# Kernel tuning notes

Measured on AMD Instinct MI355X. Metric: run time of the kernel, lower is better.

The kernel has to match this reference:

```python
import jax, jax.numpy as jnp
import numpy as np

B, T, D, H = 1024, 128, 128, 256

def _uni(k, shape, fan):
    s = 1.0 / np.sqrt(fan)
    return jax.random.uniform(k, shape, jnp.float32, -s, s)

def setup_inputs():
    key = jax.random.key(0)
    ks = jax.random.split(key, 22)
    inp = {}
    inp['x'] = jax.random.normal(ks[0], (B, T, D), jnp.float32)
    inp['x_hat'] = jax.random.normal(ks[1], (B, T, D), jnp.float32)
    inp['u'] = jax.random.uniform(ks[2], (B, T, D), jnp.float32)
    inp['m'] = (jax.random.uniform(ks[3], (B, T, D)) < 0.8).astype(jnp.float32)
    inp['d'] = jax.random.uniform(ks[4], (B, T, D), jnp.float32)
    # Decay(D -> H)
    inp['W_decay'] = _uni(ks[5], (H, D), D)
    inp['b_decay'] = _uni(ks[6], (H,), D)
    # hist: Linear(H -> D)
    inp['W_hist'] = _uni(ks[7], (D, H), H)
    inp['b_hist'] = _uni(ks[8], (D,), H)
    inp['Wv'] = _uni(ks[9], (D, D), D)
    inp['bv'] = _uni(ks[10], (D,), D)
    inp['Wr'] = _uni(ks[11], (D, D), D)
    inp['br'] = _uni(ks[12], (D,), D)
    # Conv1d(2,1,kernel=1) == learned 2-way combine
    inp['conv_w'] = _uni(ks[13], (2,), 2)
    inp['conv_b'] = _uni(ks[14], (), 2)
    # GRUCell(2*D -> H), torch layout [3H, in] rows = (r, z, n)
    inp['W_ih'] = _uni(ks[15], (3 * H, 2 * D), 2 * D)
    inp['W_hh'] = _uni(ks[16], (3 * H, H), H)
    inp['b_ih'] = _uni(ks[17], (3 * H,), H)
    inp['b_hh'] = _uni(ks[18], (3 * H,), H)
    # fc_out: Linear(H -> 1)
    inp['W_out'] = _uni(ks[19], (1, H), H)
    inp['b_out'] = _uni(ks[20], (1,), H)
    return inp

def reference(x, x_hat, u, m, d, W_decay, b_decay, W_hist, b_hist, Wv, bv, Wr, br,
              conv_w, conv_b, W_ih, W_hh, b_ih, b_hh, W_out, b_out):
    off = 1.0 - jnp.eye(D, dtype=x.dtype)
    # Precompute everything that does not depend on the recurrent state h:
    gamma = jnp.exp(-jax.nn.relu(jnp.einsum('btd,hd->bth', d, W_decay) + b_decay))  # [B,T,H]
    xbar = m * x + (1.0 - m) * x_hat
    xu = jnp.einsum('btd,ed->bte', xbar, Wv * off) + bv  # [B,T,D] (unc_flag == 0 path)
    Wr_m = Wr * off

    def step(carry, inp):
        h, loss = carry
        x_t, m_t, g_t, xu_t = inp  # [B,D],[B,D],[B,H],[B,D]
        h = h * g_t
        x_h = h @ W_hist.T + b_hist
        x_r = m_t * x_t + (1.0 - m_t) * x_h
        xr = x_r @ Wr_m.T + br
        x_comb = conv_w[0] * xu_t + conv_w[1] * xr + conv_b  # Conv1d(2,1,1)
        loss = loss + jnp.sum(jnp.abs(x_t - x_comb) * m_t) / (jnp.sum(m_t) + 1e-5)
        x_imp = m_t * x_t + (1.0 - m_t) * x_comb
        gin = jnp.concatenate([x_imp, m_t], axis=1)  # [B, 2D]
        gi = gin @ W_ih.T + b_ih
        gh = h @ W_hh.T + b_hh
        i_r, i_z, i_n = jnp.split(gi, 3, axis=1)
        h_r, h_z, h_n = jnp.split(gh, 3, axis=1)
        r = jax.nn.sigmoid(i_r + h_r)
        z = jax.nn.sigmoid(i_z + h_z)
        n = jnp.tanh(i_n + r * h_n)
        h_new = (1.0 - z) * n + z * h
        return (h_new, loss), (x_imp, xr)

    h0 = jnp.zeros((B, H), x.dtype)
    xs = (jnp.swapaxes(x, 0, 1), jnp.swapaxes(m, 0, 1),
          jnp.swapaxes(gamma, 0, 1), jnp.swapaxes(xu, 0, 1))
    (h_fin, x_loss), (x_imp_t, xr_t) = jax.lax.scan(step, (h0, jnp.float32(0.0)), xs)
    x_imp = jnp.swapaxes(x_imp_t, 0, 1)  # [B,T,D]
    xrs = jnp.swapaxes(xr_t, 0, 1)
    y_out = h_fin @ W_out.T + b_out  # task == 'C', get_y == True
    y_score = jax.nn.sigmoid(y_out)
    return (x_imp, y_out, y_score, x_loss, xu, xrs)
```

## Files before the change

### kernel.cpp

```cpp
#include <hip/hip_runtime.h>
#include <math.h>

#define BQ 1024
#define TT 128
#define DD 128
#define HH 256
#define NW 8
#define NTH 512
#define NBLK 64

typedef float f32x4 __attribute__((ext_vector_type(4)));
typedef __bf16 bf16x8 __attribute__((ext_vector_type(8)));
typedef unsigned short u16x4 __attribute__((ext_vector_type(4)));
typedef unsigned short u16x8 __attribute__((ext_vector_type(8)));
typedef unsigned int u32x4 __attribute__((ext_vector_type(4)));
typedef unsigned int u32x2 __attribute__((ext_vector_type(2)));
typedef long long i64;

#define WS_MSUMF 8192
#define WS_WQ8   40960
#define WS_WB16  487424
#define WS_SA1   589824
#define WS_SA2   67698688

#define TQ_TOT  864

#define TB_DEC 0
#define TB_WV  64
#define TB_TOT 96

#define L_WX  0
#define L_HI  98304
#define L_WR  131072
#define L_HF8 147456
#define L_XRF 151552
#define L_XIF 153600
#define L_RED 155648
#define L_TOT 155712

__device__ __forceinline__ unsigned short f2bf(float f){
  union { float f; unsigned u; } v; v.f = f;
  unsigned r = v.u + 0x7FFFu + ((v.u >> 16) & 1u);
  return (unsigned short)(r >> 16);
}
__device__ __forceinline__ float sigm(float v){ return 1.f/(1.f + __expf(-v)); }
__device__ __forceinline__ float tanhfast(float v){ return 2.f*sigm(2.f*v) - 1.f; }
__device__ __forceinline__ unsigned pk4(float a, float b, float c, float d){
  int v = __builtin_amdgcn_cvt_pk_fp8_f32(a, b, 0, false);
  v = __builtin_amdgcn_cvt_pk_fp8_f32(c, d, v, true);
  return (unsigned)v;
}
__device__ __forceinline__ f32x4 upk4(unsigned w){
  f32x4 r;
  r[0] = __builtin_amdgcn_cvt_f32_fp8((int)w, 0);
  r[1] = __builtin_amdgcn_cvt_f32_fp8((int)w, 1);
  r[2] = __builtin_amdgcn_cvt_f32_fp8((int)w, 2);
  r[3] = __builtin_amdgcn_cvt_f32_fp8((int)w, 3);
  return r;
}
__device__ __forceinline__ f32x4 mfma8(i64 a, i64 b, f32x4 c){
  return __builtin_amdgcn_mfma_f32_16x16x32_fp8_fp8(a, b, c, 0, 0, 0);
}
__device__ __forceinline__ f32x4 mfma16b(bf16x8 a, bf16x8 b, f32x4 c){
  return __builtin_amdgcn_mfma_f32_16x16x32_bf16(a, b, c, 0, 0, 0);
}

__global__ void pack_w8(const float* Whh, const float* Wih, const float* Whist,
                        const float* Wr, unsigned char* wq){
  int gt = blockIdx.x*4 + (threadIdx.x>>6);
  int lane = threadIdx.x & 63;
  if (gt >= TQ_TOT) return;
  int lr = lane & 15, lg = lane >> 4;
  const float* src; int n, k0, K; int dm = 0;
  if (gt < 384){ int kt = gt & 7, gnt = gt >> 3;
    n = (gnt>>4)*256 + (gnt&15)*16 + lr; k0 = kt*32 + lg*8; src = Whh; K = 256; }
  else if (gt < 576){ int id = gt-384; int kt = id & 3, gnt = id >> 2;
    n = (gnt>>4)*256 + (gnt&15)*16 + lr; k0 = kt*32 + lg*8; src = Wih; K = 256; }
  else if (gt < 640){ int id = gt-576; int kt = id & 7, nt = id >> 3;
    n = nt*16 + lr; k0 = kt*32 + lg*8; src = Whist; K = 256; }
  else if (gt < 672){ int id = gt-640; int kt = id & 3, nt = id >> 2;
    n = nt*16 + lr; k0 = kt*32 + lg*8; src = Wr; K = 128; dm = 1; }
  else { int id = gt-672; int kt = id & 3, gnt = id >> 2;
    n = (gnt>>4)*256 + (gnt&15)*16 + lr; k0 = 128 + kt*32 + lg*8; src = Wih; K = 256; }
  float f[8];
  #pragma unroll
  for (int e = 0; e < 8; ++e){
    int k = k0 + e;
    float v = src[(size_t)n*K + k];
    if (dm && n == k) v = 0.f;
    f[e] = v;
  }
  unsigned lo = pk4(f[0],f[1],f[2],f[3]), hi = pk4(f[4],f[5],f[6],f[7]);
  *(unsigned*)(wq + (size_t)gt*512 + lane*8) = lo;
  *(unsigned*)(wq + (size_t)gt*512 + lane*8 + 4) = hi;
}

__global__ void pack_w16(const float* Wdec, const float* Wv, unsigned short* wb){
  int gt = blockIdx.x*4 + (threadIdx.x>>6);
  int lane = threadIdx.x & 63;
  if (gt >= TB_TOT) return;
  int lr = lane & 15, lg = lane >> 4;
  const float* src; int n; int dm = 0; int kt;
  if (gt < TB_WV){ kt = gt & 3; n = (gt>>2)*16 + lr; src = Wdec; }
  else { int id = gt - TB_WV; kt = id & 3; n = (id>>2)*16 + lr; src = Wv; dm = 1; }
  int k0 = kt*32 + lg*8;
  u16x8 pkv;
  #pragma unroll
  for (int e = 0; e < 8; ++e){
    int k = k0 + e;
    float v = src[(size_t)n*128 + k];
    if (dm && n == k) v = 0.f;
    pkv[e] = f2bf(v);
  }
  *(u16x8*)(wb + (size_t)gt*512 + lane*8) = pkv;
}

__global__ void msum_kernel(const float* m, float* wsf){
  int t = blockIdx.x;
  float s = 0.f;
  for (int i = threadIdx.x; i < BQ*DD/4; i += 256){
    int b = i >> 5, c4 = (i & 31)*4;
    f32x4 v = *(const f32x4*)(m + ((size_t)b*TT + t)*DD + c4);
    s += v[0]+v[1]+v[2]+v[3];
  }
  #pragma unroll
  for (int off = 32; off >= 1; off >>= 1) s += __shfl_down(s, off);
  __shared__ float ps[4];
  if ((threadIdx.x & 63) == 0) ps[threadIdx.x >> 6] = s;
  __syncthreads();
  if (threadIdx.x == 0) wsf[WS_MSUMF + t] = ps[0] + ps[1] + ps[2] + ps[3];
}

__global__ void loss_final(const float* wsf, float* out_loss){
  __shared__ float ps[TT];
  int t = threadIdx.x;
  float s = 0.f;
  #pragma unroll 4
  for (int b = 0; b < NBLK; ++b) s += wsf[t*NBLK + b];
  ps[t] = s / (wsf[WS_MSUMF + t] + 1e-5f);
  __syncthreads();
  if (t == 0){ float a = 0.f; for (int i = 0; i < TT; ++i) a += ps[i]; *out_loss = a; }
}

__global__ __launch_bounds__(NTH, 2) void prep1_kernel(
    const float* __restrict__ x, const float* __restrict__ xhat,
    const float* __restrict__ m, const float* __restrict__ dly,
    const float* __restrict__ b_dec, const float* __restrict__ bv,
    const unsigned short* __restrict__ wb, unsigned* __restrict__ saA,
    float* __restrict__ out_xu)
{
  __shared__ __align__(16) char sm[12288];
  const int tid = threadIdx.x, w = tid>>6, lane = tid&63, lr = lane&15, lg = lane>>4;
  const int btile = blockIdx.x >> 4, tch = blockIdx.x & 15, b0 = btile*16;
  const int tg0 = tch*8;
  const int colD = w*16 + lr, colH0 = w*32 + lr;
  bf16x8 decR[2][4], wvR[4];
  #pragma unroll
  for (int s = 0; s < 2; ++s)
    #pragma unroll
    for (int kt = 0; kt < 4; ++kt)
      decR[s][kt] = *(const bf16x8*)(wb + (size_t)(TB_DEC + (w*2+s)*4 + kt)*512 + lane*8);
  #pragma unroll
  for (int kt = 0; kt < 4; ++kt)
    wvR[kt] = *(const bf16x8*)(wb + (size_t)(TB_WV + w*4 + kt)*512 + lane*8);
  const float bd0 = b_dec[colH0], bd1 = b_dec[colH0+16], bvv = bv[colD];
  const int srow = tid >> 5, c4 = (tid & 31)*4;
  const int kt_ = c4 >> 5, dl_ = ((c4 & 31) >> 3)*16 + srow, e0_ = c4 & 7;
  const size_t gbase = (size_t)(b0 + srow)*TT*DD + c4;

  f32x4 xv = *(const f32x4*)(x    + gbase + (size_t)tg0*DD);
  f32x4 hv = *(const f32x4*)(xhat + gbase + (size_t)tg0*DD);
  f32x4 mv = *(const f32x4*)(m    + gbase + (size_t)tg0*DD);
  f32x4 dv = *(const f32x4*)(dly  + gbase + (size_t)tg0*DD);

  for (int tt = 0; tt < 8; ++tt){
    int tg = tg0 + tt;
    u16x4 pd, pxb, pm;
    #pragma unroll
    for (int e = 0; e < 4; ++e){
      pd[e]  = f2bf(dv[e]);
      pxb[e] = f2bf(mv[e]*xv[e] + (1.f - mv[e])*hv[e]);
      pm[e]  = f2bf(mv[e]);
    }
    *(u16x4*)(sm + 0    + kt_*1024 + dl_*16 + e0_*2) = pd;
    *(u16x4*)(sm + 4096 + kt_*1024 + dl_*16 + e0_*2) = pxb;
    *(u16x4*)(sm + 8192 + srow*256 + c4*2) = pm;
    __syncthreads();

    {
      size_t g2 = gbase + (size_t)((tt < 7) ? tg+1 : tg)*DD;
      xv = *(const f32x4*)(x + g2);
      hv = *(const f32x4*)(xhat + g2);
      mv = *(const f32x4*)(m + g2);
      dv = *(const f32x4*)(dly + g2);
    }

    f32x4 ga0 = {0.f,0.f,0.f,0.f}, ga1 = {0.f,0.f,0.f,0.f}, xu4 = {0.f,0.f,0.f,0.f};
    #pragma unroll
    for (int kt = 0; kt < 4; ++kt){
      bf16x8 df  = *(const bf16x8*)(sm + 0    + kt*1024 + lane*16);
      bf16x8 xbf = *(const bf16x8*)(sm + 4096 + kt*1024 + lane*16);
      ga0 = mfma16b(df, decR[0][kt], ga0);
      ga1 = mfma16b(df, decR[1][kt], ga1);
      xu4 = mfma16b(xbf, wvR[kt], xu4);
    }
    float g0[4], g1[4], xuo[4];
    unsigned mask = 0;
    #pragma unroll
    for (int r = 0; r < 4; ++r){
      g0[r] = __expf(-fmaxf(ga0[r] + bd0, 0.f));
      g1[r] = __expf(-fmaxf(ga1[r] + bd1, 0.f));
      xuo[r] = xu4[r] + bvv;
      int row = lg*4 + r;
      unsigned short mu = *(const unsigned short*)(sm + 8192 + row*256 + colD*2);
      mask |= (mu ? 1u : 0u) << r;
    }
    u32x4 rec = {pk4(g0[0],g0[1],g0[2],g0[3]), pk4(g1[0],g1[1],g1[2],g1[3]),
                 pk4(xuo[0],xuo[1],xuo[2],xuo[3]), mask};
    __builtin_nontemporal_store(rec,
        (u32x4*)(saA + (((size_t)tg*NBLK + btile)*512 + tid)*4));
    #pragma unroll
    for (int r = 0; r < 4; ++r)
      __builtin_nontemporal_store(xuo[r], out_xu + ((size_t)(b0 + lg*4 + r)*TT + tg)*DD + colD);
    __syncthreads();
  }
}

__global__ __launch_bounds__(NTH, 2) void prep2_kernel(
    const float* __restrict__ m, const float* __restrict__ b_ih,
    const float* __restrict__ b_hh, const unsigned char* __restrict__ wq,
    unsigned* __restrict__ saB)
{
  __shared__ __align__(16) char sm[2048];
  const int tid = threadIdx.x, w = tid>>6, lane = tid&63, lr = lane&15, lg = lane>>4;
  const int btile = blockIdx.x >> 4, tch = blockIdx.x & 15, b0 = btile*16;
  const int tg0 = tch*8;
  i64 wihmR[6][4];
  float bfold[6];
  #pragma unroll
  for (int g = 0; g < 3; ++g)
    #pragma unroll
    for (int s = 0; s < 2; ++s){
      int j = g*2 + s;
      #pragma unroll
      for (int kt = 0; kt < 4; ++kt)
        wihmR[j][kt] = *(const i64*)(wq + (size_t)(672 + (g*16 + w*2+s)*4 + kt)*512 + lane*8);
      int n = g*256 + w*32 + s*16 + lr;
      bfold[j] = b_ih[n] + ((g < 2) ? b_hh[n] : 0.f);
    }
  const int srow = tid >> 5, c4 = (tid & 31)*4;
  const int kt_ = c4 >> 5, lg2 = (c4 & 31) >> 3, e0_ = c4 & 7;
  const size_t gbase = (size_t)(b0 + srow)*TT*DD + c4;

  for (int tt = 0; tt < 8; ++tt){
    int tg = tg0 + tt;
    f32x4 mv = *(const f32x4*)(m + gbase + (size_t)tg*DD);
    unsigned wbyte = 0;
    #pragma unroll
    for (int e = 0; e < 4; ++e) wbyte |= (mv[e] > 0.5f ? 0x38u : 0u) << (8*e);
    *(unsigned*)(sm + kt_*512 + (lg2*16 + srow)*8 + e0_) = wbyte;
    __syncthreads();

    i64 ma[4];
    #pragma unroll
    for (int kt = 0; kt < 4; ++kt) ma[kt] = *(const i64*)(sm + kt*512 + lane*8);
    f32x4 z4 = {0.f,0.f,0.f,0.f};
    f32x4 acc[6] = {z4,z4,z4,z4,z4,z4};
    #pragma unroll
    for (int j = 0; j < 6; ++j)
      #pragma unroll
      for (int kt = 0; kt < 4; ++kt)
        acc[j] = mfma8(ma[kt], wihmR[j][kt], acc[j]);
    unsigned wd[6];
    #pragma unroll
    for (int j = 0; j < 6; ++j)
      wd[j] = pk4(acc[j][0]+bfold[j], acc[j][1]+bfold[j], acc[j][2]+bfold[j], acc[j][3]+bfold[j]);
    unsigned* rp = saB + (((size_t)tg*NBLK + btile)*512 + tid)*6;
    u32x2 p0 = {wd[0], wd[1]}, p1 = {wd[2], wd[3]}, p2 = {wd[4], wd[5]};
    __builtin_nontemporal_store(p0, (u32x2*)rp);
    __builtin_nontemporal_store(p1, (u32x2*)(rp+2));
    __builtin_nontemporal_store(p2, (u32x2*)(rp+4));
    __syncthreads();
  }
}

__global__ __launch_bounds__(NTH) __attribute__((amdgpu_waves_per_eu(2, 2)))
void scan_kernel(
    const unsigned char* __restrict__ wq, const unsigned* __restrict__ saA,
    const unsigned* __restrict__ saB, const float* __restrict__ x,
    const float* __restrict__ b_hist, const float* __restrict__ br,
    const float* __restrict__ b_hh,
    const float* __restrict__ conv_w, const float* __restrict__ conv_b,
    const float* __restrict__ W_out, const float* __restrict__ b_out,
    float* __restrict__ lossP,
    float* __restrict__ out_ximp, float* __restrict__ out_y,
    float* __restrict__ out_ys, float* __restrict__ out_xrs)
{
  extern __shared__ __align__(16) char lds[];
  const int tid = threadIdx.x, w = tid>>6, lane = tid&63, lr = lane&15, lg = lane>>4;
  const int b0 = blockIdx.x*16;
  const int colD = w*16 + lr, colH0 = w*32 + lr;

  i64 whhR[3][2][8];
  #pragma unroll
  for (int g = 0; g < 3; ++g)
    #pragma unroll
    for (int s = 0; s < 2; ++s)
      #pragma unroll
      for (int kt = 0; kt < 8; ++kt)
        whhR[g][s][kt] = *(const i64*)(wq + (size_t)((g*16 + w*2+s)*8 + kt)*512 + lane*8);
  for (int i = tid; i < 9216; i += NTH)
    *(u32x4*)(lds + (size_t)i*16) = *(const u32x4*)(wq + (size_t)384*512 + (size_t)i*16);

  const float bhist_v = b_hist[colD], br_v = br[colD];
  const float bhhn0 = b_hh[512 + colH0], bhhn1 = b_hh[512 + colH0 + 16];
  const float cw0 = conv_w[0], cw1 = conv_w[1], cb = conv_b[0];

  const int hb0 = L_HF8 + w*512 + (lr>>3)*128 + lg*32 + (lr&7);
  const int f80 = (w>>1)*512 + ((w&1)*2 + (lr>>3))*128 + lg*32 + (lr&7);
  float* red = (float*)(lds + L_RED);

  float hs[2][4] = {{0.f,0.f,0.f,0.f},{0.f,0.f,0.f,0.f}};

  const unsigned* rpa = saA + ((size_t)blockIdx.x*512 + tid)*4;
  const unsigned* rpb = saB + ((size_t)blockIdx.x*512 + tid)*6;
  const size_t STA = (size_t)NBLK*512*4, STB = (size_t)NBLK*512*6;
  const float* xb = x + (size_t)(b0 + lg*4)*TT*DD + colD;

  u32x4 pfA = __builtin_nontemporal_load((const u32x4*)rpa);
  u32x2 pfB0 = __builtin_nontemporal_load((const u32x2*)rpb);
  u32x2 pfB1 = __builtin_nontemporal_load((const u32x2*)(rpb+2));
  u32x2 pfB2 = __builtin_nontemporal_load((const u32x2*)(rpb+4));
  float xc_[4];
  #pragma unroll
  for (int r = 0; r < 4; ++r) xc_[r] = xb[(size_t)r*TT*DD];

  #pragma unroll 1
  for (int t = 0; t < TT; ++t){
    const unsigned* npa = (t < TT-1) ? (rpa + STA) : rpa;
    const unsigned* npb = (t < TT-1) ? (rpb + STB) : rpb;
    int tn = (t < TT-1) ? t+1 : t;
    u32x4 nA = __builtin_nontemporal_load((const u32x4*)npa);
    u32x2 nB0 = __builtin_nontemporal_load((const u32x2*)npb);
    u32x2 nB1 = __builtin_nontemporal_load((const u32x2*)(npb+2));
    u32x2 nB2 = __builtin_nontemporal_load((const u32x2*)(npb+4));
    float xn_[4];
    #pragma unroll
    for (int r = 0; r < 4; ++r) xn_[r] = xb[(size_t)r*TT*DD + (size_t)tn*DD];

    {
      f32x4 gA0 = upk4(pfA[0]), gA1 = upk4(pfA[1]);
      #pragma unroll
      for (int r = 0; r < 4; ++r){
        hs[0][r] *= gA0[r];
        hs[1][r] *= gA1[r];
      }
    }
    unsigned q0 = pk4(hs[0][0], hs[0][1], hs[0][2], hs[0][3]);
    unsigned q1 = pk4(hs[1][0], hs[1][1], hs[1][2], hs[1][3]);
    #pragma unroll
    for (int r = 0; r < 4; ++r){
      *(unsigned char*)(lds + hb0 +       r*8) = (unsigned char)(q0 >> (8*r));
      *(unsigned char*)(lds + hb0 + 256 + r*8) = (unsigned char)(q1 >> (8*r));
    }
    __syncthreads();

    i64 ha[8];
    #pragma unroll
    for (int kt = 0; kt < 8; ++kt)
      ha[kt] = *(const i64*)(lds + L_HF8 + kt*512 + lane*8);
    f32x4 z4 = {0.f,0.f,0.f,0.f};
    f32x4 aRZ[2][2] = {{z4,z4},{z4,z4}};
    f32x4 aNh[2] = {z4,z4}, aNi[2] = {z4,z4}, xh4 = z4;
    #pragma unroll
    for (int s = 0; s < 2; ++s)
      #pragma unroll
      for (int kt = 0; kt < 8; ++kt){
        aRZ[0][s] = mfma8(ha[kt], whhR[0][s][kt], aRZ[0][s]);
        aRZ[1][s] = mfma8(ha[kt], whhR[1][s][kt], aRZ[1][s]);
        aNh[s]    = mfma8(ha[kt], whhR[2][s][kt], aNh[s]);
      }
    #pragma unroll
    for (int kt = 0; kt < 8; ++kt)
      xh4 = mfma8(ha[kt], *(const i64*)(lds + L_HI + (w*8+kt)*512 + lane*8), xh4);
    {
      unsigned mk = pfA[3];
      float x0 = (mk & 1u) ? xc_[0] : (xh4[0] + bhist_v);
      float x1 = (mk & 2u) ? xc_[1] : (xh4[1] + bhist_v);
      float x2 = (mk & 4u) ? xc_[2] : (xh4[2] + bhist_v);
      float x3 = (mk & 8u) ? xc_[3] : (xh4[3] + bhist_v);
      unsigned p = pk4(x0, x1, x2, x3);
      #pragma unroll
      for (int r = 0; r < 4; ++r)
        *(unsigned char*)(lds + L_XRF + f80 + r*8) = (unsigned char)((p >> (8*r)) & 0xff);
    }
    __syncthreads();

    f32x4 xr4 = z4;
    #pragma unroll
    for (int kt = 0; kt < 4; ++kt)
      xr4 = mfma8(*(const i64*)(lds + L_XRF + kt*512 + lane*8),
                  *(const i64*)(lds + L_WR + (w*4+kt)*512 + lane*8), xr4);
    float lpart = 0.f, xi_[4];
    unsigned mk = pfA[3];
    f32x4 xu4v = upk4(pfA[2]);
    #pragma unroll
    for (int r = 0; r < 4; ++r){
      int row = lg*4 + r;
      size_t go = ((size_t)(b0+row)*TT + t)*DD + colD;
      float xrv = xr4[r] + br_v;
      float xuv = xu4v[r];
      __builtin_nontemporal_store(xrv, out_xrs + go);
      float xc = cw0*xuv + cw1*xrv + cb;
      bool mb = (mk >> r) & 1u;
      lpart += mb ? fabsf(xc_[r] - xc) : 0.f;
      xi_[r] = mb ? xc_[r] : xc;
      __builtin_nontemporal_store(xi_[r], out_ximp + go);
    }
    {
      unsigned q = pk4(xi_[0], xi_[1], xi_[2], xi_[3]);
      #pragma unroll
      for (int r = 0; r < 4; ++r)
        *(unsigned char*)(lds + L_XIF + f80 + r*8) = (unsigned char)((q >> (8*r)) & 0xff);
    }
    #pragma unroll
    for (int off = 32; off >= 1; off >>= 1) lpart += __shfl_down(lpart, off);
    if (lane == 0) red[w] = lpart;
    __syncthreads();

    i64 xia[4];
    #pragma unroll
    for (int kt = 0; kt < 4; ++kt) xia[kt] = *(const i64*)(lds + L_XIF + kt*512 + lane*8);
    #pragma unroll
    for (int s = 0; s < 2; ++s)
      #pragma unroll
      for (int kt = 0; kt < 4; ++kt){
        aRZ[0][s] = mfma8(xia[kt], *(const i64*)(lds + L_WX + ((0*16 + w*2+s)*4 + kt)*512 + lane*8), aRZ[0][s]);
        aRZ[1][s] = mfma8(xia[kt], *(const i64*)(lds + L_WX + ((1*16 + w*2+s)*4 + kt)*512 + lane*8), aRZ[1][s]);
        aNi[s]    = mfma8(xia[kt], *(const i64*)(lds + L_WX + ((2*16 + w*2+s)*4 + kt)*512 + lane*8), aNi[s]);
      }
    if (tid == 0){
      float ssum = 0.f;
      #pragma unroll
      for (int i = 0; i < 8; ++i) ssum += red[i];
      lossP[t*NBLK + blockIdx.x] = ssum;
    }
    {
      f32x4 gR0 = upk4(pfB0[0]), gR1 = upk4(pfB0[1]);
      f32x4 gZ0 = upk4(pfB1[0]), gZ1 = upk4(pfB1[1]);
      f32x4 gN0 = upk4(pfB2[0]), gN1 = upk4(pfB2[1]);
      #pragma unroll
      for (int r = 0; r < 4; ++r){
        float rr0 = sigm(aRZ[0][0][r] + gR0[r]);
        float zz0 = sigm(aRZ[1][0][r] + gZ0[r]);
        float nn0 = tanhfast(aNi[0][r] + gN0[r] + rr0*(aNh[0][r] + bhhn0));
        hs[0][r] = (1.f - zz0)*nn0 + zz0*hs[0][r];
        float rr1 = sigm(aRZ[0][1][r] + gR1[r]);
        float zz1 = sigm(aRZ[1][1][r] + gZ1[r]);
        float nn1 = tanhfast(aNi[1][r] + gN1[r] + rr1*(aNh[1][r] + bhhn1));
        hs[1][r] = (1.f - zz1)*nn1 + zz1*hs[1][r];
      }
    }
    pfA = nA; pfB0 = nB0; pfB1 = nB1; pfB2 = nB2;
    xc_[0] = xn_[0]; xc_[1] = xn_[1]; xc_[2] = xn_[2]; xc_[3] = xn_[3];
    rpa = npa; rpb = npb;
  }

  __syncthreads();
  float* hfin = (float*)lds;
  #pragma unroll
  for (int s = 0; s < 2; ++s)
    #pragma unroll
    for (int r = 0; r < 4; ++r)
      hfin[(lg*4+r)*HH + colH0 + s*16] = hs[s][r];
  __syncthreads();
  float* psum = (float*)(lds + 16384);
  if (tid < 256){
    int row = tid >> 4, seg = tid & 15;
    float p = 0.f;
    #pragma unroll
    for (int c = 0; c < 16; ++c) p += hfin[row*HH + seg*16 + c]*W_out[seg*16 + c];
    psum[tid] = p;
  }
  __syncthreads();
  if (tid < 16){
    float yv = b_out[0];
    #pragma unroll
    for (int i = 0; i < 16; ++i) yv += psum[tid*16 + i];
    out_y[b0 + tid] = yv;
    out_ys[b0 + tid] = sigm(yv);
  }
}

extern "C" void kernel_launch(void* const* d_in, const int* in_sizes, int n_in,
                              void* d_out, int out_size, void* d_ws, size_t ws_size,
                              hipStream_t stream){
  const float* x     = (const float*)d_in[0];
  const float* xhat  = (const float*)d_in[1];
  const float* m     = (const float*)d_in[3];
  const float* dly   = (const float*)d_in[4];
  const float* Wdec  = (const float*)d_in[5];
  const float* b_dec = (const float*)d_in[6];
  const float* Whist = (const float*)d_in[7];
  const float* b_hist= (const float*)d_in[8];
  const float* Wv    = (const float*)d_in[9];
  const float* bvv   = (const float*)d_in[10];
  const float* Wr    = (const float*)d_in[11];
  const float* brr   = (const float*)d_in[12];
  const float* convw = (const float*)d_in[13];
  const float* convb = (const float*)d_in[14];
  const float* Wih   = (const float*)d_in[15];
  const float* Whh   = (const float*)d_in[16];
  const float* b_ih  = (const float*)d_in[17];
  const float* b_hh  = (const float*)d_in[18];
  const float* W_out = (const float*)d_in[19];
  const float* b_out = (const float*)d_in[20];

  float* wsf = (float*)d_ws;
  unsigned char* wq = (unsigned char*)d_ws + WS_WQ8;
  unsigned short* wb = (unsigned short*)((char*)d_ws + WS_WB16);
  unsigned* saA = (unsigned*)((char*)d_ws + WS_SA1);
  unsigned* saB = (unsigned*)((char*)d_ws + WS_SA2);

  float* out = (float*)d_out;
  size_t btd = (size_t)BQ*TT*DD;
  float* out_ximp = out;
  float* out_y    = out + btd;
  float* out_ys   = out_y + BQ;
  float* out_loss = out_ys + BQ;
  float* out_xu   = out_loss + 1;
  float* out_xrs  = out_xu + btd;

  (void)hipFuncSetAttribute((const void*)scan_kernel,
                            hipFuncAttributeMaxDynamicSharedMemorySize, L_TOT);

  pack_w8<<<TQ_TOT/4, 256, 0, stream>>>(Whh, Wih, Whist, Wr, wq);
  pack_w16<<<TB_TOT/4, 256, 0, stream>>>(Wdec, Wv, wb);
  msum_kernel<<<TT, 256, 0, stream>>>(m, wsf);
  prep1_kernel<<<1024, NTH, 0, stream>>>(x, xhat, m, dly, b_dec, bvv, wb, saA, out_xu);
  prep2_kernel<<<1024, NTH, 0, stream>>>(m, b_ih, b_hh, wq, saB);
  scan_kernel<<<NBLK, NTH, L_TOT, stream>>>(wq, saA, saB, x, b_hist, brr, b_hh,
      convw, convb, W_out, b_out, wsf,
      out_ximp, out_y, out_ys, out_xrs);
  loss_final<<<1, TT, 0, stream>>>(wsf, out_loss);
}
```

Measured before the change: 625.2 us.

## Fuse prep kernels, stage x as bf16 records, defer loss reduction to end

Merges the two precompute kernels into one so x/m are read once and the W_ih·m gate contribution is computed alongside gamma and xu. The scan kernel no longer reads strided fp32 x from global memory. It instead streams a packed bf16 copy of x laid out like the other per-step records. The per-step loss block reduction and global write are replaced by a per-thread accumulator scaled by precomputed 1/sum(m), reduced once at the end. MFMA sections are also raised in wave priority. The changes cut per-step sync and reduction work and scattered loads in the latency-bound recurrence, at the cost of rounding x to bf16 for the loss and imputation.

```diff
diff --git a/kernel.cpp b/kernel.cpp
--- a/kernel.cpp
+++ b/kernel.cpp
@@ -21,10 +21,10 @@
 #define WS_WQ8   40960
 #define WS_WB16  487424
 #define WS_SA1   589824
-#define WS_SA2   67698688
+#define WS_SAX   67698688
+#define WS_SA2   101253120
 
 #define TQ_TOT  864
-
 #define TB_DEC 0
 #define TB_WV  64
 #define TB_TOT 96
@@ -35,13 +35,17 @@
 #define L_HF8 147456
 #define L_XRF 151552
 #define L_XIF 153600
-#define L_RED 155648
-#define L_TOT 155712
+#define L_IMS 155648
+#define L_RED 156160
+#define L_TOT 156224
 
 __device__ __forceinline__ unsigned short f2bf(float f){
   union { float f; unsigned u; } v; v.f = f;
   unsigned r = v.u + 0x7FFFu + ((v.u >> 16) & 1u);
   return (unsigned short)(r >> 16);
+}
+__device__ __forceinline__ float bf2f(unsigned short u){
+  union { unsigned u; float f; } v; v.u = ((unsigned)u) << 16; return v.f;
 }
 __device__ __forceinline__ float sigm(float v){ return 1.f/(1.f + __expf(-v)); }
 __device__ __forceinline__ float tanhfast(float v){ return 2.f*sigm(2.f*v) - 1.f; }
@@ -128,28 +132,26 @@
   __shared__ float ps[4];
   if ((threadIdx.x & 63) == 0) ps[threadIdx.x >> 6] = s;
   __syncthreads();
-  if (threadIdx.x == 0) wsf[WS_MSUMF + t] = ps[0] + ps[1] + ps[2] + ps[3];
-}
-
-__global__ void loss_final(const float* wsf, float* out_loss){
-  __shared__ float ps[TT];
-  int t = threadIdx.x;
-  float s = 0.f;
-  #pragma unroll 4
-  for (int b = 0; b < NBLK; ++b) s += wsf[t*NBLK + b];
-  ps[t] = s / (wsf[WS_MSUMF + t] + 1e-5f);
-  __syncthreads();
-  if (t == 0){ float a = 0.f; for (int i = 0; i < TT; ++i) a += ps[i]; *out_loss = a; }
-}
-
-__global__ __launch_bounds__(NTH, 2) void prep1_kernel(
+  if (threadIdx.x == 0) wsf[WS_MSUMF + t] = 1.f/(ps[0]+ps[1]+ps[2]+ps[3] + 1e-5f);
+}
+
+__global__ void loss_final(const float* lossP, float* out_loss){
+  float v = lossP[threadIdx.x];
+  #pragma unroll
+  for (int off = 32; off >= 1; off >>= 1) v += __shfl_down(v, off);
+  if (threadIdx.x == 0) *out_loss = v;
+}
+
+__global__ __launch_bounds__(512, 2) void prep_kernel(
     const float* __restrict__ x, const float* __restrict__ xhat,
     const float* __restrict__ m, const float* __restrict__ dly,
     const float* __restrict__ b_dec, const float* __restrict__ bv,
-    const unsigned short* __restrict__ wb, unsigned* __restrict__ saA,
-    float* __restrict__ out_xu)
+    const float* __restrict__ b_ih, const float* __restrict__ b_hh,
+    const unsigned short* __restrict__ wb, const unsigned char* __restrict__ wq,
+    unsigned* __restrict__ saA, unsigned* __restrict__ saX,
+    unsigned* __restrict__ saB, float* __restrict__ out_xu)
 {
-  __shared__ __align__(16) char sm[12288];
+  __shared__ __align__(16) char sm[18432];
   const int tid = threadIdx.x, w = tid>>6, lane = tid&63, lr = lane&15, lg = lane>>4;
   const int btile = blockIdx.x >> 4, tch = blockIdx.x & 15, b0 = btile*16;
   const int tg0 = tch*8;
@@ -163,6 +165,19 @@
   #pragma unroll
   for (int kt = 0; kt < 4; ++kt)
     wvR[kt] = *(const bf16x8*)(wb + (size_t)(TB_WV + w*4 + kt)*512 + lane*8);
+  i64 wihmR[6][4];
+  float bfold[6];
+  #pragma unroll
+  for (int g = 0; g < 3; ++g)
+    #pragma unroll
+    for (int s = 0; s < 2; ++s){
+      int j = g*2 + s;
+      #pragma unroll
+      for (int kt = 0; kt < 4; ++kt)
+        wihmR[j][kt] = *(const i64*)(wq + (size_t)(672 + (g*16 + w*2+s)*4 + kt)*512 + lane*8);
+      int n = g*256 + w*32 + s*16 + lr;
+      bfold[j] = b_ih[n] + ((g < 2) ? b_hh[n] : 0.f);
+    }
   const float bd0 = b_dec[colH0], bd1 = b_dec[colH0+16], bvv = bv[colD];
   const int srow = tid >> 5, c4 = (tid & 31)*4;
   const int kt_ = c4 >> 5, dl_ = ((c4 & 31) >> 3)*16 + srow, e0_ = c4 & 7;
@@ -175,16 +190,21 @@
 
   for (int tt = 0; tt < 8; ++tt){
     int tg = tg0 + tt;
-    u16x4 pd, pxb, pm;
+    u16x4 pd, pxb, pm, px;
+    unsigned wbyte = 0;
     #pragma unroll
     for (int e = 0; e < 4; ++e){
       pd[e]  = f2bf(dv[e]);
       pxb[e] = f2bf(mv[e]*xv[e] + (1.f - mv[e])*hv[e]);
       pm[e]  = f2bf(mv[e]);
-    }
-    *(u16x4*)(sm + 0    + kt_*1024 + dl_*16 + e0_*2) = pd;
-    *(u16x4*)(sm + 4096 + kt_*1024 + dl_*16 + e0_*2) = pxb;
-    *(u16x4*)(sm + 8192 + srow*256 + c4*2) = pm;
+      px[e]  = f2bf(xv[e]);
+      wbyte |= (mv[e] > 0.5f ? 0x38u : 0u) << (8*e);
+    }
+    *(u16x4*)(sm + 0     + kt_*1024 + dl_*16 + e0_*2) = pd;
+    *(u16x4*)(sm + 4096  + kt_*1024 + dl_*16 + e0_*2) = pxb;
+    *(u16x4*)(sm + 8192  + srow*256 + c4*2) = pm;
+    *(unsigned*)(sm + 12288 + kt_*512 + dl_*8 + e0_) = wbyte;
+    *(u16x4*)(sm + 14336 + srow*256 + c4*2) = px;
     __syncthreads();
 
     {
@@ -195,7 +215,8 @@
       dv = *(const f32x4*)(dly + g2);
     }
 
-    f32x4 ga0 = {0.f,0.f,0.f,0.f}, ga1 = {0.f,0.f,0.f,0.f}, xu4 = {0.f,0.f,0.f,0.f};
+    f32x4 z4 = {0.f,0.f,0.f,0.f};
+    f32x4 ga0 = z4, ga1 = z4, xu4 = z4;
     #pragma unroll
     for (int kt = 0; kt < 4; ++kt){
       bf16x8 df  = *(const bf16x8*)(sm + 0    + kt*1024 + lane*16);
@@ -204,8 +225,19 @@
       ga1 = mfma16b(df, decR[1][kt], ga1);
       xu4 = mfma16b(xbf, wvR[kt], xu4);
     }
+    i64 ma[4];
+    #pragma unroll
+    for (int kt = 0; kt < 4; ++kt) ma[kt] = *(const i64*)(sm + 12288 + kt*512 + lane*8);
+    f32x4 acc[6] = {z4,z4,z4,z4,z4,z4};
+    #pragma unroll
+    for (int j = 0; j < 6; ++j)
+      #pragma unroll
+      for (int kt = 0; kt < 4; ++kt)
+        acc[j] = mfma8(ma[kt], wihmR[j][kt], acc[j]);
+
     float g0[4], g1[4], xuo[4];
     unsigned mask = 0;
+    unsigned short x16[4];
     #pragma unroll
     for (int r = 0; r < 4; ++r){
       g0[r] = __expf(-fmaxf(ga0[r] + bd0, 0.f));
@@ -213,12 +245,24 @@
       xuo[r] = xu4[r] + bvv;
       int row = lg*4 + r;
       unsigned short mu = *(const unsigned short*)(sm + 8192 + row*256 + colD*2);
+      x16[r] = *(const unsigned short*)(sm + 14336 + row*256 + colD*2);
       mask |= (mu ? 1u : 0u) << r;
     }
+    size_t recb = ((size_t)tg*NBLK + btile)*512 + tid;
     u32x4 rec = {pk4(g0[0],g0[1],g0[2],g0[3]), pk4(g1[0],g1[1],g1[2],g1[3]),
                  pk4(xuo[0],xuo[1],xuo[2],xuo[3]), mask};
-    __builtin_nontemporal_store(rec,
-        (u32x4*)(saA + (((size_t)tg*NBLK + btile)*512 + tid)*4));
+    __builtin_nontemporal_store(rec, (u32x4*)(saA + recb*4));
+    u32x2 xrec = {(unsigned)x16[0] | ((unsigned)x16[1] << 16),
+                  (unsigned)x16[2] | ((unsigned)x16[3] << 16)};
+    __builtin_nontemporal_store(xrec, (u32x2*)(saX + recb*2));
+    unsigned wd[6];
+    #pragma unroll
+    for (int j = 0; j < 6; ++j)
+      wd[j] = pk4(acc[j][0]+bfold[j], acc[j][1]+bfold[j], acc[j][2]+bfold[j], acc[j][3]+bfold[j]);
+    u32x2 p0 = {wd[0], wd[1]}, p1 = {wd[2], wd[3]}, p2 = {wd[4], wd[5]};
+    __builtin_nontemporal_store(p0, (u32x2*)(saB + recb*6));
+    __builtin_nontemporal_store(p1, (u32x2*)(saB + recb*6 + 2));
+    __builtin_nontemporal_store(p2, (u32x2*)(saB + recb*6 + 4));
     #pragma unroll
     for (int r = 0; r < 4; ++r)
       __builtin_nontemporal_store(xuo[r], out_xu + ((size_t)(b0 + lg*4 + r)*TT + tg)*DD + colD);
@@ -226,68 +270,11 @@
   }
 }
 
-__global__ __launch_bounds__(NTH, 2) void prep2_kernel(
-    const float* __restrict__ m, const float* __restrict__ b_ih,
-    const float* __restrict__ b_hh, const unsigned char* __restrict__ wq,
-    unsigned* __restrict__ saB)
-{
-  __shared__ __align__(16) char sm[2048];
-  const int tid = threadIdx.x, w = tid>>6, lane = tid&63, lr = lane&15, lg = lane>>4;
-  const int btile = blockIdx.x >> 4, tch = blockIdx.x & 15, b0 = btile*16;
-  const int tg0 = tch*8;
-  i64 wihmR[6][4];
-  float bfold[6];
-  #pragma unroll
-  for (int g = 0; g < 3; ++g)
-    #pragma unroll
-    for (int s = 0; s < 2; ++s){
-      int j = g*2 + s;
-      #pragma unroll
-      for (int kt = 0; kt < 4; ++kt)
-        wihmR[j][kt] = *(const i64*)(wq + (size_t)(672 + (g*16 + w*2+s)*4 + kt)*512 + lane*8);
-      int n = g*256 + w*32 + s*16 + lr;
-      bfold[j] = b_ih[n] + ((g < 2) ? b_hh[n] : 0.f);
-    }
-  const int srow = tid >> 5, c4 = (tid & 31)*4;
-  const int kt_ = c4 >> 5, lg2 = (c4 & 31) >> 3, e0_ = c4 & 7;
-  const size_t gbase = (size_t)(b0 + srow)*TT*DD + c4;
-
-  for (int tt = 0; tt < 8; ++tt){
-    int tg = tg0 + tt;
-    f32x4 mv = *(const f32x4*)(m + gbase + (size_t)tg*DD);
-    unsigned wbyte = 0;
-    #pragma unroll
-    for (int e = 0; e < 4; ++e) wbyte |= (mv[e] > 0.5f ? 0x38u : 0u) << (8*e);
-    *(unsigned*)(sm + kt_*512 + (lg2*16 + srow)*8 + e0_) = wbyte;
-    __syncthreads();
-
-    i64 ma[4];
-    #pragma unroll
-    for (int kt = 0; kt < 4; ++kt) ma[kt] = *(const i64*)(sm + kt*512 + lane*8);
-    f32x4 z4 = {0.f,0.f,0.f,0.f};
-    f32x4 acc[6] = {z4,z4,z4,z4,z4,z4};
-    #pragma unroll
-    for (int j = 0; j < 6; ++j)
-      #pragma unroll
-      for (int kt = 0; kt < 4; ++kt)
-        acc[j] = mfma8(ma[kt], wihmR[j][kt], acc[j]);
-    unsigned wd[6];
-    #pragma unroll
-    for (int j = 0; j < 6; ++j)
-      wd[j] = pk4(acc[j][0]+bfold[j], acc[j][1]+bfold[j], acc[j][2]+bfold[j], acc[j][3]+bfold[j]);
-    unsigned* rp = saB + (((size_t)tg*NBLK + btile)*512 + tid)*6;
-    u32x2 p0 = {wd[0], wd[1]}, p1 = {wd[2], wd[3]}, p2 = {wd[4], wd[5]};
-    __builtin_nontemporal_store(p0, (u32x2*)rp);
-    __builtin_nontemporal_store(p1, (u32x2*)(rp+2));
-    __builtin_nontemporal_store(p2, (u32x2*)(rp+4));
-    __syncthreads();
-  }
-}
-
 __global__ __launch_bounds__(NTH) __attribute__((amdgpu_waves_per_eu(2, 2)))
 void scan_kernel(
     const unsigned char* __restrict__ wq, const unsigned* __restrict__ saA,
-    const unsigned* __restrict__ saB, const float* __restrict__ x,
+    const unsigned* __restrict__ saX, const unsigned* __restrict__ saB,
+    const float* __restrict__ msumInv,
     const float* __restrict__ b_hist, const float* __restrict__ br,
     const float* __restrict__ b_hh,
     const float* __restrict__ conv_w, const float* __restrict__ conv_b,
@@ -311,6 +298,7 @@
         whhR[g][s][kt] = *(const i64*)(wq + (size_t)((g*16 + w*2+s)*8 + kt)*512 + lane*8);
   for (int i = tid; i < 9216; i += NTH)
     *(u32x4*)(lds + (size_t)i*16) = *(const u32x4*)(wq + (size_t)384*512 + (size_t)i*16);
+  if (tid < TT) *(float*)(lds + L_IMS + tid*4) = msumInv[tid];
 
   const float bhist_v = b_hist[colD], br_v = br[colD];
   const float bhhn0 = b_hh[512 + colH0], bhhn1 = b_hh[512 + colH0 + 16];
@@ -321,32 +309,30 @@
   float* red = (float*)(lds + L_RED);
 
   float hs[2][4] = {{0.f,0.f,0.f,0.f},{0.f,0.f,0.f,0.f}};
+  float lacc = 0.f;
 
   const unsigned* rpa = saA + ((size_t)blockIdx.x*512 + tid)*4;
+  const unsigned* rpx = saX + ((size_t)blockIdx.x*512 + tid)*2;
   const unsigned* rpb = saB + ((size_t)blockIdx.x*512 + tid)*6;
-  const size_t STA = (size_t)NBLK*512*4, STB = (size_t)NBLK*512*6;
-  const float* xb = x + (size_t)(b0 + lg*4)*TT*DD + colD;
+  const size_t STA = (size_t)NBLK*512*4, STX = (size_t)NBLK*512*2, STB = (size_t)NBLK*512*6;
 
   u32x4 pfA = __builtin_nontemporal_load((const u32x4*)rpa);
+  u32x2 pfX = __builtin_nontemporal_load((const u32x2*)rpx);
   u32x2 pfB0 = __builtin_nontemporal_load((const u32x2*)rpb);
   u32x2 pfB1 = __builtin_nontemporal_load((const u32x2*)(rpb+2));
   u32x2 pfB2 = __builtin_nontemporal_load((const u32x2*)(rpb+4));
-  float xc_[4];
-  #pragma unroll
-  for (int r = 0; r < 4; ++r) xc_[r] = xb[(size_t)r*TT*DD];
+  __syncthreads();
 
   #pragma unroll 1
   for (int t = 0; t < TT; ++t){
     const unsigned* npa = (t < TT-1) ? (rpa + STA) : rpa;
+    const unsigned* npx = (t < TT-1) ? (rpx + STX) : rpx;
     const unsigned* npb = (t < TT-1) ? (rpb + STB) : rpb;
-    int tn = (t < TT-1) ? t+1 : t;
     u32x4 nA = __builtin_nontemporal_load((const u32x4*)npa);
+    u32x2 nX = __builtin_nontemporal_load((const u32x2*)npx);
     u32x2 nB0 = __builtin_nontemporal_load((const u32x2*)npb);
     u32x2 nB1 = __builtin_nontemporal_load((const u32x2*)(npb+2));
     u32x2 nB2 = __builtin_nontemporal_load((const u32x2*)(npb+4));
-    float xn_[4];
-    #pragma unroll
-    for (int r = 0; r < 4; ++r) xn_[r] = xb[(size_t)r*TT*DD + (size_t)tn*DD];
 
     {
       f32x4 gA0 = upk4(pfA[0]), gA1 = upk4(pfA[1]);
@@ -372,6 +358,7 @@
     f32x4 z4 = {0.f,0.f,0.f,0.f};
     f32x4 aRZ[2][2] = {{z4,z4},{z4,z4}};
     f32x4 aNh[2] = {z4,z4}, aNi[2] = {z4,z4}, xh4 = z4;
+    __builtin_amdgcn_s_setprio(1);
     #pragma unroll
     for (int s = 0; s < 2; ++s)
       #pragma unroll
@@ -383,12 +370,17 @@
     #pragma unroll
     for (int kt = 0; kt < 8; ++kt)
       xh4 = mfma8(ha[kt], *(const i64*)(lds + L_HI + (w*8+kt)*512 + lane*8), xh4);
+    __builtin_amdgcn_s_setprio(0);
     {
       unsigned mk = pfA[3];
-      float x0 = (mk & 1u) ? xc_[0] : (xh4[0] + bhist_v);
-      float x1 = (mk & 2u) ? xc_[1] : (xh4[1] + bhist_v);
-      float x2 = (mk & 4u) ? xc_[2] : (xh4[2] + bhist_v);
-      float x3 = (mk & 8u) ? xc_[3] : (xh4[3] + bhist_v);
+      float xf0 = bf2f((unsigned short)(pfX[0] & 0xffffu));
+      float xf1 = bf2f((unsigned short)(pfX[0] >> 16));
+      float xf2 = bf2f((unsigned short)(pfX[1] & 0xffffu));
+      float xf3 = bf2f((unsigned short)(pfX[1] >> 16));
+      float x0 = (mk & 1u) ? xf0 : (xh4[0] + bhist_v);
+      float x1 = (mk & 2u) ? xf1 : (xh4[1] + bhist_v);
+      float x2 = (mk & 4u) ? xf2 : (xh4[2] + bhist_v);
+      float x3 = (mk & 8u) ? xf3 : (xh4[3] + bhist_v);
       unsigned p = pk4(x0, x1, x2, x3);
       #pragma unroll
       for (int r = 0; r < 4; ++r)
@@ -397,40 +389,46 @@
     __syncthreads();
 
     f32x4 xr4 = z4;
+    __builtin_amdgcn_s_setprio(1);
     #pragma unroll
     for (int kt = 0; kt < 4; ++kt)
       xr4 = mfma8(*(const i64*)(lds + L_XRF + kt*512 + lane*8),
                   *(const i64*)(lds + L_WR + (w*4+kt)*512 + lane*8), xr4);
-    float lpart = 0.f, xi_[4];
-    unsigned mk = pfA[3];
-    f32x4 xu4v = upk4(pfA[2]);
-    #pragma unroll
-    for (int r = 0; r < 4; ++r){
-      int row = lg*4 + r;
-      size_t go = ((size_t)(b0+row)*TT + t)*DD + colD;
-      float xrv = xr4[r] + br_v;
-      float xuv = xu4v[r];
-      __builtin_nontemporal_store(xrv, out_xrs + go);
-      float xc = cw0*xuv + cw1*xrv + cb;
-      bool mb = (mk >> r) & 1u;
-      lpart += mb ? fabsf(xc_[r] - xc) : 0.f;
-      xi_[r] = mb ? xc_[r] : xc;
-      __builtin_nontemporal_store(xi_[r], out_ximp + go);
-    }
+    __builtin_amdgcn_s_setprio(0);
     {
+      unsigned mk = pfA[3];
+      f32x4 xu4v = upk4(pfA[2]);
+      float xf_[4];
+      xf_[0] = bf2f((unsigned short)(pfX[0] & 0xffffu));
+      xf_[1] = bf2f((unsigned short)(pfX[0] >> 16));
+      xf_[2] = bf2f((unsigned short)(pfX[1] & 0xffffu));
+      xf_[3] = bf2f((unsigned short)(pfX[1] >> 16));
+      float ims = *(const float*)(lds + L_IMS + t*4);
+      float lp = 0.f, xi_[4];
+      #pragma unroll
+      for (int r = 0; r < 4; ++r){
+        int row = lg*4 + r;
+        size_t go = ((size_t)(b0+row)*TT + t)*DD + colD;
+        float xrv = xr4[r] + br_v;
+        __builtin_nontemporal_store(xrv, out_xrs + go);
+        float xc = cw0*xu4v[r] + cw1*xrv + cb;
+        bool mb = (mk >> r) & 1u;
+        lp += mb ? fabsf(xf_[r] - xc) : 0.f;
+        xi_[r] = mb ? xf_[r] : xc;
+        __builtin_nontemporal_store(xi_[r], out_ximp + go);
+      }
+      lacc += lp * ims;
       unsigned q = pk4(xi_[0], xi_[1], xi_[2], xi_[3]);
       #pragma unroll
       for (int r = 0; r < 4; ++r)
         *(unsigned char*)(lds + L_XIF + f80 + r*8) = (unsigned char)((q >> (8*r)) & 0xff);
     }
-    #pragma unroll
-    for (int off = 32; off >= 1; off >>= 1) lpart += __shfl_down(lpart, off);
-    if (lane == 0) red[w] = lpart;
     __syncthreads();
 
     i64 xia[4];
     #pragma unroll
     for (int kt = 0; kt < 4; ++kt) xia[kt] = *(const i64*)(lds + L_XIF + kt*512 + lane*8);
+    __builtin_amdgcn_s_setprio(1);
     #pragma unroll
     for (int s = 0; s < 2; ++s)
       #pragma unroll
@@ -439,12 +437,7 @@
         aRZ[1][s] = mfma8(xia[kt], *(const i64*)(lds + L_WX + ((1*16 + w*2+s)*4 + kt)*512 + lane*8), aRZ[1][s]);
         aNi[s]    = mfma8(xia[kt], *(const i64*)(lds + L_WX + ((2*16 + w*2+s)*4 + kt)*512 + lane*8), aNi[s]);
       }
-    if (tid == 0){
-      float ssum = 0.f;
-      #pragma unroll
-      for (int i = 0; i < 8; ++i) ssum += red[i];
-      lossP[t*NBLK + blockIdx.x] = ssum;
-    }
+    __builtin_amdgcn_s_setprio(0);
     {
       f32x4 gR0 = upk4(pfB0[0]), gR1 = upk4(pfB0[1]);
       f32x4 gZ0 = upk4(pfB1[0]), gZ1 = upk4(pfB1[1]);
@@ -461,12 +454,14 @@
         hs[1][r] = (1.f - zz1)*nn1 + zz1*hs[1][r];
       }
     }
-    pfA = nA; pfB0 = nB0; pfB1 = nB1; pfB2 = nB2;
-    xc_[0] = xn_[0]; xc_[1] = xn_[1]; xc_[2] = xn_[2]; xc_[3] = xn_[3];
-    rpa = npa; rpb = npb;
+    pfA = nA; pfX = nX; pfB0 = nB0; pfB1 = nB1; pfB2 = nB2;
+    rpa = npa; rpx = npx; rpb = npb;
   }
 
   __syncthreads();
+  #pragma unroll
+  for (int off = 32; off >= 1; off >>= 1) lacc += __shfl_down(lacc, off);
+  if (lane == 0) red[w] = lacc;
   float* hfin = (float*)lds;
   #pragma unroll
   for (int s = 0; s < 2; ++s)
@@ -474,6 +469,12 @@
     for (int r = 0; r < 4; ++r)
       hfin[(lg*4+r)*HH + colH0 + s*16] = hs[s][r];
   __syncthreads();
+  if (tid == 0){
+    float s = 0.f;
+    #pragma unroll
+    for (int i = 0; i < NW; ++i) s += red[i];
+    lossP[blockIdx.x] = s;
+  }
   float* psum = (float*)(lds + 16384);
   if (tid < 256){
     int row = tid >> 4, seg = tid & 15;
@@ -520,6 +521,7 @@
   unsigned char* wq = (unsigned char*)d_ws + WS_WQ8;
   unsigned short* wb = (unsigned short*)((char*)d_ws + WS_WB16);
   unsigned* saA = (unsigned*)((char*)d_ws + WS_SA1);
+  unsigned* saX = (unsigned*)((char*)d_ws + WS_SAX);
   unsigned* saB = (unsigned*)((char*)d_ws + WS_SA2);
 
   float* out = (float*)d_out;
@@ -537,10 +539,10 @@
   pack_w8<<<TQ_TOT/4, 256, 0, stream>>>(Whh, Wih, Whist, Wr, wq);
   pack_w16<<<TB_TOT/4, 256, 0, stream>>>(Wdec, Wv, wb);
   msum_kernel<<<TT, 256, 0, stream>>>(m, wsf);
-  prep1_kernel<<<1024, NTH, 0, stream>>>(x, xhat, m, dly, b_dec, bvv, wb, saA, out_xu);
-  prep2_kernel<<<1024, NTH, 0, stream>>>(m, b_ih, b_hh, wq, saB);
-  scan_kernel<<<NBLK, NTH, L_TOT, stream>>>(wq, saA, saB, x, b_hist, brr, b_hh,
-      convw, convb, W_out, b_out, wsf,
+  prep_kernel<<<1024, 512, 0, stream>>>(x, xhat, m, dly, b_dec, bvv, b_ih, b_hh,
+      wb, wq, saA, saX, saB, out_xu);
+  scan_kernel<<<NBLK, NTH, L_TOT, stream>>>(wq, saA, saX, saB, wsf + WS_MSUMF,
+      b_hist, brr, b_hh, convw, convb, W_out, b_out, wsf,
       out_ximp, out_y, out_ys, out_xrs);
-  loss_final<<<1, TT, 0, stream>>>(wsf, out_loss);
-}
+  loss_final<<<1, 64, 0, stream>>>(wsf, out_loss);
+}
```

Result: no change. 624.9 us (-0.0%).
